# Kernel optimization log

Measured on AMD Instinct MI355X. Metric: run time of the kernel, lower is better.

Reference implementation:

```python
import jax, jax.numpy as jnp
import numpy as np

B, C, L, N = 2, 8, 128, 48  # volume side L, kept size N per axis (fact=4 -> N >= L/4)


def setup_inputs() -> dict:
    key = jax.random.key(0)
    ks = jax.random.split(key, 7)
    x = jax.random.normal(ks[0], (B, C, L, L, L), dtype=jnp.float32)
    EN3 = jax.random.normal(ks[1], (L, N), dtype=jnp.float32)
    EN2 = jax.random.normal(ks[2], (L, N), dtype=jnp.float32)
    EN1 = jax.random.normal(ks[3], (L, N), dtype=jnp.float32)
    DE3 = jax.random.normal(ks[4], (N, L), dtype=jnp.float32)
    DE2 = jax.random.normal(ks[5], (N, L), dtype=jnp.float32)
    DE1 = jax.random.normal(ks[6], (N, L), dtype=jnp.float32)
    return {"x": x, "EN3": EN3, "EN2": EN2, "EN1": EN1,
            "DE3": DE3, "DE2": DE2, "DE1": DE1}


def reference(x, EN3, EN2, EN1, DE3, DE2, DE1):
    # ---- encode: contract D (axis -3) with EN3, H (axis -2) with EN2, W (axis -1) with EN1
    e = jnp.einsum('bcdhw,dp->bcphw', x, EN3)
    e = jnp.einsum('bcphw,hq->bcpqw', e, EN2)
    enc = jnp.einsum('bcpqw,wr->bcpqr', e, EN1)  # (B,C,N,N,N)
    # ---- decode: three application orders of DE1/DE2/DE3, averaged (as in source)
    # order W,H,D
    y = jnp.einsum('bcpqr,rw->bcpqw', enc, DE1)
    y = jnp.einsum('bcpqw,qh->bcphw', y, DE2)
    y1 = jnp.einsum('bcphw,pd->bcdhw', y, DE3)
    # order H,D,W
    y = jnp.einsum('bcpqr,qh->bcphr', enc, DE2)
    y = jnp.einsum('bcphr,pd->bcdhr', y, DE3)
    y2 = jnp.einsum('bcdhr,rw->bcdhw', y, DE1)
    # order D,W,H
    y = jnp.einsum('bcpqr,pd->bcdqr', enc, DE3)
    y = jnp.einsum('bcdqr,rw->bcdqw', y, DE1)
    y3 = jnp.einsum('bcdqw,qh->bcdhw', y, DE2)
    return (y1 + y2 + y3) / 3.0
```

## Files before the change

### kernel.cpp

```cpp
#include <hip/hip_runtime.h>


#define LDIM 128
#define NDIM 48
#define HW   (LDIM * LDIM)
#define L3V  (LDIM * HW)

typedef __bf16 bf16x8 __attribute__((ext_vector_type(8)));
typedef float  f32x4  __attribute__((ext_vector_type(4)));
typedef unsigned short u16;

#define S128 136
#define S64  72

#define W_EN3T 0
#define W_EN2T 6144
#define W_EN1T 12288
#define W_DE3T 18432
#define W_DE2T 26624
#define W_DE1T 34816
#define W_TOT  43008

__device__ __forceinline__ u16 f2bf(float f) {
    unsigned int u = __builtin_bit_cast(unsigned int, f);
    return (u16)((u + 0x7fffu + ((u >> 16) & 1u)) >> 16);
}
__device__ __forceinline__ bf16x8 frag(const u16* p) {
    return *reinterpret_cast<const bf16x8*>(p);
}
__device__ __forceinline__ f32x4 mfma16(bf16x8 a, bf16x8 b, f32x4 c) {
    return __builtin_amdgcn_mfma_f32_16x16x32_bf16(a, b, c, 0, 0, 0);
}

__global__ __launch_bounds__(256) void kPrep(const float* __restrict__ EN3,
                                             const float* __restrict__ EN2,
                                             const float* __restrict__ EN1,
                                             const float* __restrict__ DE3,
                                             const float* __restrict__ DE2,
                                             const float* __restrict__ DE1,
                                             u16* __restrict__ W) {
    int i = blockIdx.x * 256 + threadIdx.x;
    if (i < 6144)       { int p = i >> 7, d = i & 127;                 W[i] = f2bf(EN3[d * 48 + p]); }
    else if (i < 12288) { int j = i - 6144;  int q = j >> 7, h = j & 127; W[i] = f2bf(EN2[h * 48 + q]); }
    else if (i < 18432) { int j = i - 12288; int r = j >> 7, w = j & 127; W[i] = f2bf(EN1[w * 48 + r]); }
    else if (i < 26624) { int j = i - 18432; int d = j >> 6, p = j & 63;  W[i] = f2bf(p < 48 ? DE3[p * 128 + d] : 0.f); }
    else if (i < 34816) { int j = i - 26624; int h = j >> 6, q = j & 63;  W[i] = f2bf(q < 48 ? DE2[q * 128 + h] : 0.f); }
    else if (i < 43008) { int j = i - 34816; int w = j >> 6, r = j & 63;  W[i] = f2bf(r < 48 ? DE1[r * 128 + w] : 0.f); }
}

__global__ __launch_bounds__(256) void kA(const float* __restrict__ x,
                                          const u16* __restrict__ W,
                                          u16* __restrict__ t1) {
    __shared__ u16 lx[128 * S128];
    __shared__ u16 lo[48 * S128];
    const int bc  = blockIdx.y;
    const int hw0 = blockIdx.x * 128;
    const int t = threadIdx.x, lane = t & 63, wv = t >> 6, quad = lane >> 4;

    bf16x8 afr[3][4];
    {
        const int row = lane & 15, kof = quad * 8;
        for (int m = 0; m < 3; ++m)
            for (int kk = 0; kk < 4; ++kk)
                afr[m][kk] = frag(W + W_EN3T + (m * 16 + row) * 128 + kk * 32 + kof);
    }
    {
        const int d   = t & 127;
        const int hwg = (t >> 7) * 64;
        const float* xp = x + (size_t)bc * L3V + (size_t)d * HW + hw0 + hwg;
        for (int i = 0; i < 16; ++i) {
            float4 v = *reinterpret_cast<const float4*>(xp + i * 4);
            int n = hwg + i * 4;
            lx[(n + 0) * S128 + d] = f2bf(v.x);
            lx[(n + 1) * S128 + d] = f2bf(v.y);
            lx[(n + 2) * S128 + d] = f2bf(v.z);
            lx[(n + 3) * S128 + d] = f2bf(v.w);
        }
    }
    __syncthreads();
    f32x4 acc[3][2] = {};
    {
        const int n0 = wv * 32, brow = lane & 15, bkof = quad * 8;
        for (int kk = 0; kk < 4; ++kk) {
            bf16x8 b0 = frag(lx + (n0 + brow) * S128 + kk * 32 + bkof);
            bf16x8 b1 = frag(lx + (n0 + 16 + brow) * S128 + kk * 32 + bkof);
            for (int m = 0; m < 3; ++m) {
                acc[m][0] = mfma16(afr[m][kk], b0, acc[m][0]);
                acc[m][1] = mfma16(afr[m][kk], b1, acc[m][1]);
            }
        }
    }
    {
        const int n0 = wv * 32, col = lane & 15;
        for (int m = 0; m < 3; ++m)
            for (int nf = 0; nf < 2; ++nf)
                for (int r = 0; r < 4; ++r) {
                    int p = m * 16 + quad * 4 + r;
                    int n = n0 + nf * 16 + col;
                    lo[p * S128 + n] = f2bf(acc[m][nf][r]);
                }
    }
    __syncthreads();
    u16* op = t1 + (size_t)(bc * 48) * HW + hw0;
    for (int i = 0; i < 3; ++i) {
        int idx = t + i * 256;
        int p = idx >> 4, c = (idx & 15) * 8;
        *reinterpret_cast<float4*>(op + (size_t)p * HW + c) =
            *reinterpret_cast<const float4*>(lo + p * S128 + c);
    }
}

__global__ __launch_bounds__(256) void kMid(const u16* __restrict__ t1,
                                            const u16* __restrict__ W,
                                            u16* __restrict__ u2) {
    __shared__ u16 pool[26624];
    u16* lT = pool;
    u16* lE = pool + 6528;
    u16* lO = pool;
    u16* lU = pool + 17408;

    const int slab = blockIdx.x;
    const int t = threadIdx.x, lane = t & 63, wv = t >> 6, quad = lane >> 4;
    const int row = lane & 15, kof = quad * 8;
    const u16* Sg = t1 + (size_t)slab * HW;

    for (int i = t; i < 48 * 16; i += 256)  { int q = i >> 4; lE[q * S64 + 48 + (i & 15)] = 0; }
    for (int i = t; i < 128 * 16; i += 256) { int w = i >> 4; lU[w * S64 + 48 + (i & 15)] = 0; }

    {
        const int h0 = wv * 32;
        f32x4 acc[2][3] = {};
        for (int kk = 0; kk < 4; ++kk) {
            bf16x8 b[3];
            for (int n = 0; n < 3; ++n)
                b[n] = frag(W + W_EN1T + (n * 16 + row) * 128 + kk * 32 + kof);
            for (int m = 0; m < 2; ++m) {
                bf16x8 a = frag(Sg + (h0 + m * 16 + row) * 128 + kk * 32 + kof);
                for (int n = 0; n < 3; ++n) acc[m][n] = mfma16(a, b[n], acc[m][n]);
            }
        }
        for (int m = 0; m < 2; ++m)
            for (int n = 0; n < 3; ++n) {
                int r = n * 16 + row;
                int h = h0 + m * 16 + quad * 4;
                uint2 pk;
                pk.x = (unsigned)f2bf(acc[m][n][0]) | ((unsigned)f2bf(acc[m][n][1]) << 16);
                pk.y = (unsigned)f2bf(acc[m][n][2]) | ((unsigned)f2bf(acc[m][n][3]) << 16);
                *reinterpret_cast<uint2*>(lT + r * S128 + h) = pk;
            }
    }
    __syncthreads();
    if (wv < 3) {
        const int q0 = wv * 16;
        f32x4 acc[3] = {};
        for (int kk = 0; kk < 4; ++kk) {
            bf16x8 a = frag(W + W_EN2T + (q0 + row) * 128 + kk * 32 + kof);
            for (int n = 0; n < 3; ++n) {
                bf16x8 b = frag(lT + (n * 16 + row) * S128 + kk * 32 + kof);
                acc[n] = mfma16(a, b, acc[n]);
            }
        }
        for (int n = 0; n < 3; ++n)
            for (int j = 0; j < 4; ++j)
                lE[(q0 + quad * 4 + j) * S64 + n * 16 + row] = f2bf(acc[n][j]);
    }
    __syncthreads();
    {
        const int w0 = wv * 32;
        f32x4 acc[2][3] = {};
        for (int kk = 0; kk < 2; ++kk) {
            bf16x8 b[3];
            for (int n = 0; n < 3; ++n)
                b[n] = frag(lE + (n * 16 + row) * S64 + kk * 32 + kof);
            for (int m = 0; m < 2; ++m) {
                bf16x8 a = frag(W + W_DE1T + (w0 + m * 16 + row) * 64 + kk * 32 + kof);
                for (int n = 0; n < 3; ++n) acc[m][n] = mfma16(a, b[n], acc[m][n]);
            }
        }
        for (int m = 0; m < 2; ++m)
            for (int n = 0; n < 3; ++n)
                for (int j = 0; j < 4; ++j)
                    lU[(w0 + m * 16 + quad * 4 + j) * S64 + n * 16 + row] = f2bf(acc[m][n][j]);
    }
    __syncthreads();
    {
        const int m0 = (wv & 1) * 64, n0 = (wv >> 1) * 64;
        f32x4 acc[4][4] = {};
        for (int kk = 0; kk < 2; ++kk) {
            bf16x8 b[4];
            for (int n = 0; n < 4; ++n)
                b[n] = frag(lU + (n0 + n * 16 + row) * S64 + kk * 32 + kof);
            for (int m = 0; m < 4; ++m) {
                bf16x8 a = frag(W + W_DE2T + (m0 + m * 16 + row) * 64 + kk * 32 + kof);
                for (int n = 0; n < 4; ++n) acc[m][n] = mfma16(a, b[n], acc[m][n]);
            }
        }
        for (int m = 0; m < 4; ++m)
            for (int n = 0; n < 4; ++n)
                for (int j = 0; j < 4; ++j)
                    lO[(m0 + m * 16 + quad * 4 + j) * S128 + n0 + n * 16 + row] = f2bf(acc[m][n][j]);
    }
    __syncthreads();
    u16* up = u2 + (size_t)slab * HW;
    for (int i = 0; i < 8; ++i) {
        int idx = t + i * 256;
        int h = idx >> 4, c = (idx & 15) * 8;
        *reinterpret_cast<float4*>(up + h * 128 + c) =
            *reinterpret_cast<const float4*>(lO + h * S128 + c);
    }
}

__global__ __launch_bounds__(256) void kF(const u16* __restrict__ u2,
                                          const u16* __restrict__ W,
                                          float* __restrict__ out) {
    __shared__ u16 lb[128 * S64];
    const int bc = blockIdx.y, hw0 = blockIdx.x * 128;
    const int t = threadIdx.x, lane = t & 63, wv = t >> 6, quad = lane >> 4;
    const int row = lane & 15, kof = quad * 8;
    const int m0 = (wv & 1) * 64, n0 = (wv >> 1) * 64;

    bf16x8 afr[4][2];
    for (int m = 0; m < 4; ++m)
        for (int kk = 0; kk < 2; ++kk)
            afr[m][kk] = frag(W + W_DE3T + (m0 + m * 16 + row) * 64 + kk * 32 + kof);

    {
        const int p   = t & 63;
        const int hwb = (t >> 6) * 32;
        const u16* sp = u2 + ((size_t)(bc * 48) + p) * HW + hw0 + hwb;
        const bool valid = p < 48;
        for (int i = 0; i < 4; ++i) {
            u16 v[8] = {0, 0, 0, 0, 0, 0, 0, 0};
            if (valid) *reinterpret_cast<float4*>(v) = *reinterpret_cast<const float4*>(sp + i * 8);
            for (int j = 0; j < 8; ++j) lb[(hwb + i * 8 + j) * S64 + p] = v[j];
        }
    }
    __syncthreads();
    f32x4 acc[4][4] = {};
    for (int kk = 0; kk < 2; ++kk) {
        bf16x8 b[4];
        for (int n = 0; n < 4; ++n)
            b[n] = frag(lb + (n0 + n * 16 + row) * S64 + kk * 32 + kof);
        for (int m = 0; m < 4; ++m)
            for (int n = 0; n < 4; ++n) acc[m][n] = mfma16(afr[m][kk], b[n], acc[m][n]);
    }
    float* ob = out + (size_t)bc * L3V + hw0;
    for (int m = 0; m < 4; ++m)
        for (int n = 0; n < 4; ++n)
            for (int j = 0; j < 4; ++j) {
                int d = m0 + m * 16 + quad * 4 + j;
                int c = n0 + n * 16 + row;
                ob[(size_t)d * HW + c] = acc[m][n][j];
            }
}

extern "C" void kernel_launch(void* const* d_in, const int* in_sizes, int n_in,
                              void* d_out, int out_size, void* d_ws, size_t ws_size,
                              hipStream_t stream) {
    const float* x   = (const float*)d_in[0];
    const float* EN3 = (const float*)d_in[1];
    const float* EN2 = (const float*)d_in[2];
    const float* EN1 = (const float*)d_in[3];
    const float* DE3 = (const float*)d_in[4];
    const float* DE2 = (const float*)d_in[5];
    const float* DE1 = (const float*)d_in[6];
    float* out = (float*)d_out;

    u16* t1 = (u16*)d_ws;
    u16* u2 = (u16*)((char*)d_ws + 25165824);
    u16* W  = (u16*)((char*)d_ws + 50331648);

    kPrep<<<dim3(168),     256, 0, stream>>>(EN3, EN2, EN1, DE3, DE2, DE1, W);
    kA   <<<dim3(128, 16), 256, 0, stream>>>(x, W, t1);
    kMid <<<dim3(768),     256, 0, stream>>>(t1, W, u2);
    kF   <<<dim3(128, 16), 256, 0, stream>>>(u2, W, out);
}
```

Before: 279.7 us.

## Reorder contraction axes so first and last passes contract W with contiguous rows

Changes the order of separable contractions. Kernel A now contracts W (the contiguous axis) first over one D-slice per block. The middle kernel does H/D encode and H/D decode, and the final kernel applies DE1 along W and writes output rows. This replaces the transposing LDS stores and strided gathers of x with packed row-wise stores, and gives the final kernel contiguous output writes along W. The tradeoff is that the t1 and u2 intermediates are written with strided patterns of their own.

New measurement: 283.4 us. About the same (+1.3%).

```diff
diff --git a/kernel.cpp b/kernel.cpp
--- a/kernel.cpp
+++ b/kernel.cpp
@@ -52,62 +52,45 @@
                                           const u16* __restrict__ W,
                                           u16* __restrict__ t1) {
     __shared__ u16 lx[128 * S128];
-    __shared__ u16 lo[48 * S128];
-    const int bc  = blockIdx.y;
-    const int hw0 = blockIdx.x * 128;
+    const int bc = blockIdx.y;
+    const int d  = blockIdx.x;
     const int t = threadIdx.x, lane = t & 63, wv = t >> 6, quad = lane >> 4;
-
-    bf16x8 afr[3][4];
-    {
-        const int row = lane & 15, kof = quad * 8;
-        for (int m = 0; m < 3; ++m)
-            for (int kk = 0; kk < 4; ++kk)
-                afr[m][kk] = frag(W + W_EN3T + (m * 16 + row) * 128 + kk * 32 + kof);
-    }
-    {
-        const int d   = t & 127;
-        const int hwg = (t >> 7) * 64;
-        const float* xp = x + (size_t)bc * L3V + (size_t)d * HW + hw0 + hwg;
+    const int row = lane & 15, kof = quad * 8;
+
+    {
+        const float* xp = x + (size_t)bc * L3V + (size_t)d * HW;
         for (int i = 0; i < 16; ++i) {
-            float4 v = *reinterpret_cast<const float4*>(xp + i * 4);
-            int n = hwg + i * 4;
-            lx[(n + 0) * S128 + d] = f2bf(v.x);
-            lx[(n + 1) * S128 + d] = f2bf(v.y);
-            lx[(n + 2) * S128 + d] = f2bf(v.z);
-            lx[(n + 3) * S128 + d] = f2bf(v.w);
-        }
-    }
-    __syncthreads();
-    f32x4 acc[3][2] = {};
-    {
-        const int n0 = wv * 32, brow = lane & 15, bkof = quad * 8;
-        for (int kk = 0; kk < 4; ++kk) {
-            bf16x8 b0 = frag(lx + (n0 + brow) * S128 + kk * 32 + bkof);
-            bf16x8 b1 = frag(lx + (n0 + 16 + brow) * S128 + kk * 32 + bkof);
-            for (int m = 0; m < 3; ++m) {
-                acc[m][0] = mfma16(afr[m][kk], b0, acc[m][0]);
-                acc[m][1] = mfma16(afr[m][kk], b1, acc[m][1]);
-            }
-        }
-    }
-    {
-        const int n0 = wv * 32, col = lane & 15;
-        for (int m = 0; m < 3; ++m)
-            for (int nf = 0; nf < 2; ++nf)
-                for (int r = 0; r < 4; ++r) {
-                    int p = m * 16 + quad * 4 + r;
-                    int n = n0 + nf * 16 + col;
-                    lo[p * S128 + n] = f2bf(acc[m][nf][r]);
-                }
-    }
-    __syncthreads();
-    u16* op = t1 + (size_t)(bc * 48) * HW + hw0;
-    for (int i = 0; i < 3; ++i) {
-        int idx = t + i * 256;
-        int p = idx >> 4, c = (idx & 15) * 8;
-        *reinterpret_cast<float4*>(op + (size_t)p * HW + c) =
-            *reinterpret_cast<const float4*>(lo + p * S128 + c);
-    }
+            int f = i * 1024 + t * 4;
+            float4 v = *reinterpret_cast<const float4*>(xp + f);
+            int h = f >> 7, w = f & 127;
+            uint2 pk;
+            pk.x = (unsigned)f2bf(v.x) | ((unsigned)f2bf(v.y) << 16);
+            pk.y = (unsigned)f2bf(v.z) | ((unsigned)f2bf(v.w) << 16);
+            *reinterpret_cast<uint2*>(lx + h * S128 + w) = pk;
+        }
+    }
+    __syncthreads();
+    const int h0 = wv * 32;
+    f32x4 acc[2][3] = {};
+    for (int kk = 0; kk < 4; ++kk) {
+        bf16x8 b[3];
+        for (int n = 0; n < 3; ++n)
+            b[n] = frag(W + W_EN1T + (n * 16 + row) * 128 + kk * 32 + kof);
+        for (int m = 0; m < 2; ++m) {
+            bf16x8 a = frag(lx + (h0 + m * 16 + row) * S128 + kk * 32 + kof);
+            for (int n = 0; n < 3; ++n) acc[m][n] = mfma16(a, b[n], acc[m][n]);
+        }
+    }
+    u16* op = t1 + (size_t)bc * 48 * HW + d * 128;
+    for (int m = 0; m < 2; ++m)
+        for (int n = 0; n < 3; ++n) {
+            int r = n * 16 + row;
+            int h = h0 + m * 16 + quad * 4;
+            uint2 pk;
+            pk.x = (unsigned)f2bf(acc[m][n][0]) | ((unsigned)f2bf(acc[m][n][1]) << 16);
+            pk.y = (unsigned)f2bf(acc[m][n][2]) | ((unsigned)f2bf(acc[m][n][3]) << 16);
+            *reinterpret_cast<uint2*>(op + (size_t)r * HW + h) = pk;
+        }
 }
 
 __global__ __launch_bounds__(256) void kMid(const u16* __restrict__ t1,
@@ -124,37 +107,37 @@
     const int row = lane & 15, kof = quad * 8;
     const u16* Sg = t1 + (size_t)slab * HW;
 
-    for (int i = t; i < 48 * 16; i += 256)  { int q = i >> 4; lE[q * S64 + 48 + (i & 15)] = 0; }
-    for (int i = t; i < 128 * 16; i += 256) { int w = i >> 4; lU[w * S64 + 48 + (i & 15)] = 0; }
-
-    {
-        const int h0 = wv * 32;
+    for (int i = t; i < 48 * 16; i += 256)  { int p = i >> 4; lE[p * S64 + 48 + (i & 15)] = 0; }
+    for (int i = t; i < 128 * 16; i += 256) { int h = i >> 4; lU[h * S64 + 48 + (i & 15)] = 0; }
+
+    {
+        const int d0 = wv * 32;
         f32x4 acc[2][3] = {};
         for (int kk = 0; kk < 4; ++kk) {
             bf16x8 b[3];
             for (int n = 0; n < 3; ++n)
-                b[n] = frag(W + W_EN1T + (n * 16 + row) * 128 + kk * 32 + kof);
+                b[n] = frag(W + W_EN2T + (n * 16 + row) * 128 + kk * 32 + kof);
             for (int m = 0; m < 2; ++m) {
-                bf16x8 a = frag(Sg + (h0 + m * 16 + row) * 128 + kk * 32 + kof);
+                bf16x8 a = frag(Sg + (d0 + m * 16 + row) * 128 + kk * 32 + kof);
                 for (int n = 0; n < 3; ++n) acc[m][n] = mfma16(a, b[n], acc[m][n]);
             }
         }
         for (int m = 0; m < 2; ++m)
             for (int n = 0; n < 3; ++n) {
-                int r = n * 16 + row;
-                int h = h0 + m * 16 + quad * 4;
+                int q = n * 16 + row;
+                int dd = d0 + m * 16 + quad * 4;
                 uint2 pk;
                 pk.x = (unsigned)f2bf(acc[m][n][0]) | ((unsigned)f2bf(acc[m][n][1]) << 16);
                 pk.y = (unsigned)f2bf(acc[m][n][2]) | ((unsigned)f2bf(acc[m][n][3]) << 16);
-                *reinterpret_cast<uint2*>(lT + r * S128 + h) = pk;
+                *reinterpret_cast<uint2*>(lT + q * S128 + dd) = pk;
             }
     }
     __syncthreads();
     if (wv < 3) {
-        const int q0 = wv * 16;
+        const int p0 = wv * 16;
         f32x4 acc[3] = {};
         for (int kk = 0; kk < 4; ++kk) {
-            bf16x8 a = frag(W + W_EN2T + (q0 + row) * 128 + kk * 32 + kof);
+            bf16x8 a = frag(W + W_EN3T + (p0 + row) * 128 + kk * 32 + kof);
             for (int n = 0; n < 3; ++n) {
                 bf16x8 b = frag(lT + (n * 16 + row) * S128 + kk * 32 + kof);
                 acc[n] = mfma16(a, b, acc[n]);
@@ -162,25 +145,25 @@
         }
         for (int n = 0; n < 3; ++n)
             for (int j = 0; j < 4; ++j)
-                lE[(q0 + quad * 4 + j) * S64 + n * 16 + row] = f2bf(acc[n][j]);
-    }
-    __syncthreads();
-    {
-        const int w0 = wv * 32;
+                lE[(p0 + quad * 4 + j) * S64 + n * 16 + row] = f2bf(acc[n][j]);
+    }
+    __syncthreads();
+    {
+        const int h0 = wv * 32;
         f32x4 acc[2][3] = {};
         for (int kk = 0; kk < 2; ++kk) {
             bf16x8 b[3];
             for (int n = 0; n < 3; ++n)
                 b[n] = frag(lE + (n * 16 + row) * S64 + kk * 32 + kof);
             for (int m = 0; m < 2; ++m) {
-                bf16x8 a = frag(W + W_DE1T + (w0 + m * 16 + row) * 64 + kk * 32 + kof);
+                bf16x8 a = frag(W + W_DE2T + (h0 + m * 16 + row) * 64 + kk * 32 + kof);
                 for (int n = 0; n < 3; ++n) acc[m][n] = mfma16(a, b[n], acc[m][n]);
             }
         }
         for (int m = 0; m < 2; ++m)
             for (int n = 0; n < 3; ++n)
                 for (int j = 0; j < 4; ++j)
-                    lU[(w0 + m * 16 + quad * 4 + j) * S64 + n * 16 + row] = f2bf(acc[m][n][j]);
+                    lU[(h0 + m * 16 + quad * 4 + j) * S64 + n * 16 + row] = f2bf(acc[m][n][j]);
     }
     __syncthreads();
     {
@@ -191,7 +174,7 @@
             for (int n = 0; n < 4; ++n)
                 b[n] = frag(lU + (n0 + n * 16 + row) * S64 + kk * 32 + kof);
             for (int m = 0; m < 4; ++m) {
-                bf16x8 a = frag(W + W_DE2T + (m0 + m * 16 + row) * 64 + kk * 32 + kof);
+                bf16x8 a = frag(W + W_DE3T + (m0 + m * 16 + row) * 64 + kk * 32 + kof);
                 for (int n = 0; n < 4; ++n) acc[m][n] = mfma16(a, b[n], acc[m][n]);
             }
         }
@@ -214,43 +197,43 @@
                                           const u16* __restrict__ W,
                                           float* __restrict__ out) {
     __shared__ u16 lb[128 * S64];
-    const int bc = blockIdx.y, hw0 = blockIdx.x * 128;
+    const int bc = blockIdx.y, dh0 = blockIdx.x * 128;
     const int t = threadIdx.x, lane = t & 63, wv = t >> 6, quad = lane >> 4;
     const int row = lane & 15, kof = quad * 8;
     const int m0 = (wv & 1) * 64, n0 = (wv >> 1) * 64;
 
-    bf16x8 afr[4][2];
-    for (int m = 0; m < 4; ++m)
+    bf16x8 bfr[4][2];
+    for (int n = 0; n < 4; ++n)
         for (int kk = 0; kk < 2; ++kk)
-            afr[m][kk] = frag(W + W_DE3T + (m0 + m * 16 + row) * 64 + kk * 32 + kof);
-
-    {
-        const int p   = t & 63;
-        const int hwb = (t >> 6) * 32;
-        const u16* sp = u2 + ((size_t)(bc * 48) + p) * HW + hw0 + hwb;
-        const bool valid = p < 48;
+            bfr[n][kk] = frag(W + W_DE1T + (n0 + n * 16 + row) * 64 + kk * 32 + kof);
+
+    {
+        const int r   = t & 63;
+        const int dhb = (t >> 6) * 32;
+        const u16* sp = u2 + ((size_t)(bc * 48) + r) * HW + dh0 + dhb;
+        const bool valid = r < 48;
         for (int i = 0; i < 4; ++i) {
             u16 v[8] = {0, 0, 0, 0, 0, 0, 0, 0};
             if (valid) *reinterpret_cast<float4*>(v) = *reinterpret_cast<const float4*>(sp + i * 8);
-            for (int j = 0; j < 8; ++j) lb[(hwb + i * 8 + j) * S64 + p] = v[j];
+            for (int j = 0; j < 8; ++j) lb[(dhb + i * 8 + j) * S64 + r] = v[j];
         }
     }
     __syncthreads();
     f32x4 acc[4][4] = {};
     for (int kk = 0; kk < 2; ++kk) {
-        bf16x8 b[4];
-        for (int n = 0; n < 4; ++n)
-            b[n] = frag(lb + (n0 + n * 16 + row) * S64 + kk * 32 + kof);
+        bf16x8 a[4];
         for (int m = 0; m < 4; ++m)
-            for (int n = 0; n < 4; ++n) acc[m][n] = mfma16(afr[m][kk], b[n], acc[m][n]);
-    }
-    float* ob = out + (size_t)bc * L3V + hw0;
+            a[m] = frag(lb + (m0 + m * 16 + row) * S64 + kk * 32 + kof);
+        for (int m = 0; m < 4; ++m)
+            for (int n = 0; n < 4; ++n) acc[m][n] = mfma16(a[m], bfr[n][kk], acc[m][n]);
+    }
+    float* ob = out + (size_t)bc * L3V + (size_t)dh0 * 128;
     for (int m = 0; m < 4; ++m)
         for (int n = 0; n < 4; ++n)
             for (int j = 0; j < 4; ++j) {
-                int d = m0 + m * 16 + quad * 4 + j;
-                int c = n0 + n * 16 + row;
-                ob[(size_t)d * HW + c] = acc[m][n][j];
+                int dh = m0 + m * 16 + quad * 4 + j;
+                int wp = n0 + n * 16 + row;
+                ob[(size_t)dh * 128 + wp] = acc[m][n][j];
             }
 }
 
```
